# Performance work log

Hardware: AMD Instinct MI355X
Metric: run time of the kernel (lower is better)

The kernel has to match this reference:

```python
import jax, jax.numpy as jnp
import numpy as np

V = 32000   # vocab_size
D = 1024    # dim
NH = 16     # n_heads
HD = 64     # head_dim
L = 2       # n_layers
E = 8       # n_experts
K = 2       # n_active_experts
H = 2048    # expert_dim
B = 2
T = 1024
EPS = 1e-6
THETA = 10000.0
STD = 0.02


def rmsnorm(x, w):
    rms = jax.lax.rsqrt(jnp.mean(x * x, axis=-1, keepdims=True) + EPS)
    return x * rms * w


def rope_cos_sin(t_len):
    inv = 1.0 / (THETA ** (jnp.arange(0, HD, 2, dtype=jnp.float32) / HD))
    t = jnp.arange(t_len, dtype=jnp.float32)
    f = jnp.outer(t, inv)  # [T, HD//2]
    return jnp.cos(f), jnp.sin(f)


def apply_rope(x, cos, sin):
    # x: [B, T, NH, HD]; complex rotation on interleaved (even, odd) pairs
    xr = x[..., 0::2]
    xi = x[..., 1::2]
    c = cos[None, :, None, :]
    s = sin[None, :, None, :]
    out_r = xr * c - xi * s
    out_i = xr * s + xi * c
    return jnp.stack([out_r, out_i], axis=-1).reshape(x.shape)


def setup_inputs() -> dict:
    key = jax.random.key(0)
    ks = jax.random.split(key, 13)
    n = lambda k, shp: (jax.random.normal(k, shp, dtype=jnp.float32) * STD)
    return {
        "tokens": jax.random.randint(ks[0], (B, T), 0, V, dtype=jnp.int64)
                   if jax.config.jax_enable_x64 else
                   jax.random.randint(ks[0], (B, T), 0, V, dtype=jnp.int32),
        "emb": n(ks[1], (V, D)),            # tied embedding / output projection
        "attn_norm_w": jnp.ones((L, D), jnp.float32),
        "wq": n(ks[2], (L, D, D)),
        "wk": n(ks[3], (L, D, D)),
        "wv": n(ks[4], (L, D, D)),
        "wo": n(ks[5], (L, D, D)),
        "ffn_norm_w": jnp.ones((L, D), jnp.float32),
        "gate_w": n(ks[6], (L, D, E)),
        "w1": n(ks[7], (L, E, D, H)),
        "w2": n(ks[8], (L, E, H, D)),
        "w3": n(ks[9], (L, E, D, H)),
        "final_norm_w": jnp.ones((D,), jnp.float32),
    }


def reference(tokens, emb, attn_norm_w, wq, wk, wv, wo, ffn_norm_w,
              gate_w, w1, w2, w3, final_norm_w):
    b, t = tokens.shape
    h = emb[tokens]                                     # [B,T,D]
    cos, sin = rope_cos_sin(t)
    mask = jnp.where(jnp.tril(jnp.ones((t, t), bool)), 0.0, -jnp.inf)
    scale = 1.0 / np.sqrt(HD).astype(np.float32)
    aux_total = jnp.float32(0.0)

    for l in range(L):
        x = h
        # --- attention ---
        hn = rmsnorm(x, attn_norm_w[l])
        q = (hn @ wq[l]).reshape(b, t, NH, HD)
        k = (hn @ wk[l]).reshape(b, t, NH, HD)
        v = (hn @ wv[l]).reshape(b, t, NH, HD)
        q = apply_rope(q, cos, sin)
        k = apply_rope(k, cos, sin)
        scores = jnp.einsum('bqhd,bkhd->bhqk', q, k) * scale + mask
        attn = jax.nn.softmax(scores, axis=-1)
        o = jnp.einsum('bhqk,bkhd->bqhd', attn, v).reshape(b, t, D) @ wo[l]
        x = x + o
        # --- MoE ---
        xf = rmsnorm(x, ffn_norm_w[l]).reshape(-1, D)   # [N,D]
        gate_logits = xf @ gate_w[l]                    # [N,E]
        probs = jax.nn.softmax(gate_logits, axis=-1)
        vals, idx = jax.lax.top_k(probs, K)             # [N,K]
        w = vals / (jnp.sum(vals, axis=-1, keepdims=True) + 1e-8)
        oh = jax.nn.one_hot(idx, E, dtype=jnp.float32)  # [N,K,E]
        combine = jnp.sum(oh * w[..., None], axis=1)    # [N,E]
        tokens_per_expert = oh.sum(axis=1).mean(axis=0)
        aux_total = aux_total + E * jnp.sum(tokens_per_expert * probs.mean(axis=0))
        h1 = jnp.einsum('nd,edh->neh', xf, w1[l])
        h3 = jnp.einsum('nd,edh->neh', xf, w3[l])
        eo = jnp.einsum('neh,ehd->ned', jax.nn.silu(h1) * h3, w2[l])
        moe_out = jnp.einsum('ned,ne->nd', eo, combine).reshape(b, t, D)
        h = x + moe_out

    logits = rmsnorm(h, final_norm_w) @ emb.T           # [B,T,V]
    return logits, aux_total
```

## Files before the change

kernel.cpp:

```cpp
#include <hip/hip_runtime.h>
#include <hip/hip_bf16.h>
#include <math.h>

#define D_MODEL 1024
#define NHEADS  16
#define HDIM    64
#define NEXP    8
#define FFH     2048
#define BATCH   2
#define SEQ     1024
#define NTOK    2048
#define VOCAB   32000
#define LDSS    40

typedef __attribute__((ext_vector_type(4))) float f32x4;
typedef __attribute__((ext_vector_type(2))) float f32x2;
typedef __attribute__((ext_vector_type(8))) _Float16 f16x8;
typedef __attribute__((ext_vector_type(4))) unsigned short u16x4;

#define TIER    4.8828125e-4f
#define DESCALE 2.44140625e-4f
#define INV_S   0.015625f
#define INV_M   7.62939453125e-6f

__device__ __forceinline__ unsigned short f2h(float x) {
    _Float16 h = (_Float16)x;
    union { _Float16 h; unsigned short u; } v; v.h = h; return v.u;
}
__device__ __forceinline__ float h2f(unsigned short u) {
    union { unsigned short u; _Float16 h; } v; v.u = u; return (float)v.h;
}
__device__ __forceinline__ void split2h(float x, unsigned short& h, unsigned short& m) {
    _Float16 hf = (_Float16)(x * 64.f);
    union { _Float16 h; unsigned short u; } a; a.h = hf;
    h = a.u;
    float r = x - (float)hf * INV_S;
    _Float16 mf = (_Float16)(r * 131072.f);
    union { _Float16 h; unsigned short u; } b; b.h = mf;
    m = b.u;
}

#define MFMAH(a, b, c) __builtin_amdgcn_mfma_f32_16x16x32_f16((a), (b), (c), 0, 0, 0)

#define PSA ((long)NTOK * D_MODEL)
#define PSW ((long)D_MODEL * D_MODEL)

__global__ __launch_bounds__(256) void rmsnorm_kernel(const float* __restrict__ x,
    const float* __restrict__ wt, unsigned short* __restrict__ out2)
{
    __shared__ float red[4];
    int n = blockIdx.x;
    int c = threadIdx.x << 2;
    f32x4 v = *(const f32x4*)(x + (long)n*D_MODEL + c);
    float ss = v.x*v.x + v.y*v.y + v.z*v.z + v.w*v.w;
    #pragma unroll
    for (int dd = 32; dd; dd >>= 1) ss += __shfl_xor(ss, dd);
    if ((threadIdx.x & 63) == 0) red[threadIdx.x >> 6] = ss;
    __syncthreads();
    float tot = red[0] + red[1] + red[2] + red[3];
    float rms = rsqrtf(tot * (1.f / D_MODEL) + 1e-6f);
    f32x4 wv = *(const f32x4*)(wt + c);
    f32x4 o = v * rms;
    o = o * wv;
    u16x4 hv, mv;
    #pragma unroll
    for (int j = 0; j < 4; j++) { unsigned short h,m; split2h(o[j],h,m); hv[j]=h; mv[j]=m; }
    long idx = (long)n*D_MODEL + c;
    *(u16x4*)(out2 + 0*PSA + idx) = hv;
    *(u16x4*)(out2 + 1*PSA + idx) = mv;
}

__global__ __launch_bounds__(256) void wsplitT_kernel(
    const float* __restrict__ wqs, const float* __restrict__ wks, const float* __restrict__ wvs,
    unsigned short* __restrict__ oq, unsigned short* __restrict__ ok, unsigned short* __restrict__ ov)
{
    __shared__ float t[64][65];
    int k0 = blockIdx.x*64, n0 = blockIdx.y*64, z = blockIdx.z;
    const float* src = (z==0) ? wqs : (z==1) ? wks : wvs;
    unsigned short* dst = (z==0) ? oq : (z==1) ? ok : ov;
    int tid = threadIdx.x;
    int a = tid & 63, g = tid >> 6;
    #pragma unroll 4
    for (int i = 0; i < 16; i++) {
        int k = g*16 + i;
        t[k][a] = src[(long)(k0+k)*D_MODEL + n0 + a];
    }
    __syncthreads();
    #pragma unroll 4
    for (int i = 0; i < 16; i++) {
        int n = g*16 + i;
        float v = t[a][n];
        unsigned short h,m; split2h(v,h,m);
        long idx = (long)(n0+n)*D_MODEL + k0 + a;
        dst[0*PSW + idx] = h;
        dst[1*PSW + idx] = m;
    }
}

__global__ __launch_bounds__(256, 4) void qkv_kernel(
    const unsigned short* __restrict__ A2,
    const unsigned short* __restrict__ Wq2, const unsigned short* __restrict__ Wk2,
    const unsigned short* __restrict__ Wv2,
    float* __restrict__ qf, float* __restrict__ kf, float* __restrict__ vf)
{
    __shared__ __align__(16) unsigned short As[2][64*LDSS];
    __shared__ __align__(16) unsigned short Bs[2][64*LDSS];
    int z = blockIdx.z;
    const unsigned short* B2 = (z==0) ? Wq2 : (z==1) ? Wk2 : Wv2;
    float* out = (z==0) ? qf : (z==1) ? kf : vf;
    int n0 = blockIdx.x*64, m0 = blockIdx.y*64;
    int tid = threadIdx.x, w = tid >> 6, lane = tid & 63;
    int wm = (w >> 1)*32, wn = (w & 1)*32;
    int lr = lane & 15, lg = lane >> 4;
    f32x4 zero = {0.f,0.f,0.f,0.f};
    f32x4 a0[2][2], a1[2][2];
    #pragma unroll
    for (int mi = 0; mi < 2; mi++)
        #pragma unroll
        for (int ni = 0; ni < 2; ni++) { a0[mi][ni] = zero; a1[mi][ni] = zero; }
    int rb = tid >> 3, kc = (tid & 7) << 2;

    for (int k0 = 0; k0 < D_MODEL; k0 += 32) {
        #pragma unroll
        for (int p = 0; p < 2; p++) {
            int r = p*32 + rb;
            #pragma unroll
            for (int s = 0; s < 2; s++) {
                *(u16x4*)&As[s][r*LDSS + kc] = *(const u16x4*)(A2 + s*PSA + (long)(m0+r)*D_MODEL + k0 + kc);
                *(u16x4*)&Bs[s][r*LDSS + kc] = *(const u16x4*)(B2 + s*PSW + (long)(n0+r)*D_MODEL + k0 + kc);
            }
        }
        __syncthreads();
        f16x8 bh[2], bm[2];
        #pragma unroll
        for (int ni = 0; ni < 2; ni++) {
            bh[ni] = *(const f16x8*)&Bs[0][(wn + ni*16 + lr)*LDSS + lg*8];
            bm[ni] = *(const f16x8*)&Bs[1][(wn + ni*16 + lr)*LDSS + lg*8];
        }
        #pragma unroll
        for (int mi = 0; mi < 2; mi++) {
            f16x8 ah = *(const f16x8*)&As[0][(wm + mi*16 + lr)*LDSS + lg*8];
            f16x8 am = *(const f16x8*)&As[1][(wm + mi*16 + lr)*LDSS + lg*8];
            #pragma unroll
            for (int ni = 0; ni < 2; ni++) {
                a0[mi][ni] = MFMAH(ah, bh[ni], a0[mi][ni]);
                a1[mi][ni] = MFMAH(ah, bm[ni], a1[mi][ni]);
                a1[mi][ni] = MFMAH(am, bh[ni], a1[mi][ni]);
            }
        }
        __syncthreads();
    }
    #pragma unroll
    for (int mi = 0; mi < 2; mi++)
        #pragma unroll
        for (int r = 0; r < 4; r++) {
            long row = m0 + wm + mi*16 + lg*4 + r;
            #pragma unroll
            for (int ni = 0; ni < 2; ni++) {
                int col = n0 + wn + ni*16 + lr;
                out[row*D_MODEL + col] = (a0[mi][ni][r] + a1[mi][ni][r]*TIER) * DESCALE;
            }
        }
}

__global__ __launch_bounds__(256, 3) void wo_kernel(
    const float* __restrict__ A, const float* __restrict__ B, float* h)
{
    __shared__ __align__(16) unsigned short As[2][64*LDSS];
    __shared__ __align__(16) unsigned short Bs[2][64*LDSS];
    int n0 = blockIdx.x*64, m0 = blockIdx.y*64;
    int tid = threadIdx.x, w = tid >> 6, lane = tid & 63;
    int wm = (w >> 1)*32, wn = (w & 1)*32;
    int lr = lane & 15, lg = lane >> 4;
    f32x4 zero = {0.f,0.f,0.f,0.f};
    f32x4 a0[2][2], a1[2][2];
    #pragma unroll
    for (int mi = 0; mi < 2; mi++)
        #pragma unroll
        for (int ni = 0; ni < 2; ni++) { a0[mi][ni] = zero; a1[mi][ni] = zero; }
    int rb = tid >> 3, kc = (tid & 7) << 2;
    int nb = (tid & 31) << 1, kb = (tid >> 5) << 2;

    f32x4 pAv[2];
    f32x2 pBv[4];
    #pragma unroll
    for (int p = 0; p < 2; p++)
        pAv[p] = *(const f32x4*)(A + (long)(m0 + p*32 + rb)*D_MODEL + kc);
    #pragma unroll
    for (int i = 0; i < 4; i++)
        pBv[i] = *(const f32x2*)(B + (long)(kb + i)*D_MODEL + n0 + nb);

    for (int k0 = 0; k0 < D_MODEL; k0 += 32) {
        int kn = k0 + 32;
        #pragma unroll
        for (int p = 0; p < 2; p++) {
            int r = p*32 + rb;
            u16x4 hv, mv;
            #pragma unroll
            for (int j = 0; j < 4; j++) { unsigned short hh,mm; split2h(pAv[p][j],hh,mm); hv[j]=hh; mv[j]=mm; }
            *(u16x4*)&As[0][r*LDSS + kc] = hv;
            *(u16x4*)&As[1][r*LDSS + kc] = mv;
        }
        #pragma unroll
        for (int i = 0; i < 2; i++) {
            int r = nb + i;
            u16x4 hv, mv;
            unsigned short hh,mm;
            split2h(pBv[0][i],hh,mm); hv[0]=hh; mv[0]=mm;
            split2h(pBv[1][i],hh,mm); hv[1]=hh; mv[1]=mm;
            split2h(pBv[2][i],hh,mm); hv[2]=hh; mv[2]=mm;
            split2h(pBv[3][i],hh,mm); hv[3]=hh; mv[3]=mm;
            *(u16x4*)&Bs[0][r*LDSS + kb] = hv;
            *(u16x4*)&Bs[1][r*LDSS + kb] = mv;
        }
        if (kn < D_MODEL) {
            #pragma unroll
            for (int p = 0; p < 2; p++)
                pAv[p] = *(const f32x4*)(A + (long)(m0 + p*32 + rb)*D_MODEL + kn + kc);
            #pragma unroll
            for (int i = 0; i < 4; i++)
                pBv[i] = *(const f32x2*)(B + (long)(kn + kb + i)*D_MODEL + n0 + nb);
        }
        __syncthreads();
        f16x8 bh[2], bm[2];
        #pragma unroll
        for (int ni = 0; ni < 2; ni++) {
            bh[ni] = *(const f16x8*)&Bs[0][(wn + ni*16 + lr)*LDSS + lg*8];
            bm[ni] = *(const f16x8*)&Bs[1][(wn + ni*16 + lr)*LDSS + lg*8];
        }
        #pragma unroll
        for (int mi = 0; mi < 2; mi++) {
            f16x8 ah = *(const f16x8*)&As[0][(wm + mi*16 + lr)*LDSS + lg*8];
            f16x8 am = *(const f16x8*)&As[1][(wm + mi*16 + lr)*LDSS + lg*8];
            #pragma unroll
            for (int ni = 0; ni < 2; ni++) {
                a0[mi][ni] = MFMAH(ah, bh[ni], a0[mi][ni]);
                a1[mi][ni] = MFMAH(ah, bm[ni], a1[mi][ni]);
                a1[mi][ni] = MFMAH(am, bh[ni], a1[mi][ni]);
            }
        }
        __syncthreads();
    }
    #pragma unroll
    for (int mi = 0; mi < 2; mi++)
        #pragma unroll
        for (int r = 0; r < 4; r++) {
            long row = m0 + wm + mi*16 + lg*4 + r;
            #pragma unroll
            for (int ni = 0; ni < 2; ni++) {
                int col = n0 + wn + ni*16 + lr;
                h[row*D_MODEL + col] += (a0[mi][ni][r] + a1[mi][ni][r]*TIER) * DESCALE;
            }
        }
}

template<int SPL>
__global__ __launch_bounds__(256, 3) void moe13_kernel(
    const unsigned short* __restrict__ A2, const float* __restrict__ W1,
    const float* __restrict__ W3, float* __restrict__ G,
    const int* __restrict__ rowidx, const int* __restrict__ counts,
    const int* __restrict__ offsets)
{
    __shared__ __align__(16) unsigned short As[SPL][64*LDSS];
    __shared__ __align__(16) unsigned short Bs[SPL][128*LDSS];
    const int P1 = (SPL == 2) ? 1 : 0;
    int e = blockIdx.z;
    int cnt = counts[e], off = offsets[e];
    int n0 = blockIdx.x*128, m0 = blockIdx.y*64;
    if (m0 >= cnt) return;
    int tid = threadIdx.x, w = tid >> 6, lane = tid & 63;
    int wm = (w >> 1)*32, wn = (w & 1)*64;
    int lr = lane & 15, lg = lane >> 4;
    int rb = tid >> 3, kc = (tid & 7) << 2;
    f32x4 zero = {0.f,0.f,0.f,0.f};

    long arow[2]; int av[2];
    #pragma unroll
    for (int p = 0; p < 2; p++) {
        int r = p*32 + rb;
        av[p] = (m0 + r < cnt) ? 1 : 0;
        arow[p] = av[p] ? (long)rowidx[off + m0 + r] : 0;
    }
    u16x4 z4 = {0,0,0,0};
    f32x4 sl[2][4];

    #pragma unroll
    for (int mat = 0; mat < 2; mat++) {
        const float* bp = (mat ? W3 : W1) + (long)e * (D_MODEL*FFH);
        f32x4 a0[2][4], a1t[2][4];
        #pragma unroll
        for (int mi = 0; mi < 2; mi++)
            #pragma unroll
            for (int ni = 0; ni < 4; ni++) { a0[mi][ni] = zero; a1t[mi][ni] = zero; }

        for (int k0 = 0; k0 < D_MODEL; k0 += 32) {
            #pragma unroll
            for (int p = 0; p < 2; p++) {
                int r = p*32 + rb;
                #pragma unroll
                for (int s = 0; s < SPL; s++)
                    *(u16x4*)&As[s][r*LDSS + kc] = av[p] ?
                        *(const u16x4*)(A2 + s*PSA + arow[p]*D_MODEL + k0 + kc) : z4;
            }
            f32x4 c0 = *(const f32x4*)(bp + (long)(k0+kc+0)*FFH + n0 + rb*4);
            f32x4 c1 = *(const f32x4*)(bp + (long)(k0+kc+1)*FFH + n0 + rb*4);
            f32x4 c2 = *(const f32x4*)(bp + (long)(k0+kc+2)*FFH + n0 + rb*4);
            f32x4 c3 = *(const f32x4*)(bp + (long)(k0+kc+3)*FFH + n0 + rb*4);
            #pragma unroll
            for (int i = 0; i < 4; i++) {
                int r = rb*4 + i;
                if (SPL == 2) {
                    u16x4 hv, mv;
                    unsigned short hh,mm;
                    split2h(c0[i],hh,mm); hv[0]=hh; mv[0]=mm;
                    split2h(c1[i],hh,mm); hv[1]=hh; mv[1]=mm;
                    split2h(c2[i],hh,mm); hv[2]=hh; mv[2]=mm;
                    split2h(c3[i],hh,mm); hv[3]=hh; mv[3]=mm;
                    *(u16x4*)&Bs[0][r*LDSS + kc] = hv;
                    *(u16x4*)&Bs[P1][r*LDSS + kc] = mv;
                } else {
                    u16x4 hv = {f2h(c0[i]), f2h(c1[i]), f2h(c2[i]), f2h(c3[i])};
                    *(u16x4*)&Bs[0][r*LDSS + kc] = hv;
                }
            }
            __syncthreads();
            f16x8 bh[4], bm[4];
            #pragma unroll
            for (int ni = 0; ni < 4; ni++) {
                bh[ni] = *(const f16x8*)&Bs[0][(wn + ni*16 + lr)*LDSS + lg*8];
                if (SPL == 2) bm[ni] = *(const f16x8*)&Bs[P1][(wn + ni*16 + lr)*LDSS + lg*8];
            }
            #pragma unroll
            for (int mi = 0; mi < 2; mi++) {
                f16x8 ah = *(const f16x8*)&As[0][(wm + mi*16 + lr)*LDSS + lg*8];
                #pragma unroll
                for (int ni = 0; ni < 4; ni++) {
                    a0[mi][ni] = MFMAH(ah, bh[ni], a0[mi][ni]);
                    if (SPL == 2) {
                        f16x8 am = *(const f16x8*)&As[P1][(wm + mi*16 + lr)*LDSS + lg*8];
                        a1t[mi][ni] = MFMAH(ah, bm[ni], a1t[mi][ni]);
                        a1t[mi][ni] = MFMAH(am, bh[ni], a1t[mi][ni]);
                    }
                }
            }
            __syncthreads();
        }
        if (mat == 0) {
            #pragma unroll
            for (int mi = 0; mi < 2; mi++)
                #pragma unroll
                for (int ni = 0; ni < 4; ni++) {
                    f32x4 v = (SPL == 2) ? (a0[mi][ni] + a1t[mi][ni]*TIER)*DESCALE
                                         : a0[mi][ni]*INV_S;
                    #pragma unroll
                    for (int r = 0; r < 4; r++) {
                        float s = v[r];
                        v[r] = s / (1.f + expf(-s));
                    }
                    sl[mi][ni] = v;
                }
        } else {
            #pragma unroll
            for (int mi = 0; mi < 2; mi++)
                #pragma unroll
                for (int r = 0; r < 4; r++) {
                    int rowl = wm + mi*16 + lg*4 + r;
                    if (m0 + rowl < cnt) {
                        long crow = off + m0 + rowl;
                        #pragma unroll
                        for (int ni = 0; ni < 4; ni++) {
                            int col = n0 + wn + ni*16 + lr;
                            float v3 = (SPL == 2) ? (a0[mi][ni][r] + a1t[mi][ni][r]*TIER)*DESCALE
                                                  : a0[mi][ni][r]*INV_S;
                            G[crow*FFH + col] = sl[mi][ni][r] * v3;
                        }
                    }
                }
        }
    }
}

template<int SPL>
__global__ __launch_bounds__(256, 4) void w2_kernel(
    const float* __restrict__ G, const float* __restrict__ W2, float* h,
    const int* __restrict__ rowidx, const float* __restrict__ wrow,
    const int* __restrict__ counts, const int* __restrict__ offsets)
{
    __shared__ __align__(16) unsigned short As[SPL][64*LDSS];
    __shared__ __align__(16) unsigned short Bs[SPL][64*LDSS];
    const int P1 = (SPL == 2) ? 1 : 0;
    int e = blockIdx.z;
    int cnt = counts[e], off = offsets[e];
    int n0 = blockIdx.x*64, m0 = blockIdx.y*64;
    if (m0 >= cnt) return;
    const float* bp = W2 + (long)e * (FFH*D_MODEL);
    int tid = threadIdx.x, w = tid >> 6, lane = tid & 63;
    int wm = (w >> 1)*32, wn = (w & 1)*32;
    int lr = lane & 15, lg = lane >> 4;
    f32x4 zero = {0.f,0.f,0.f,0.f};
    f32x4 a0[2][2], a1[2][2];
    #pragma unroll
    for (int mi = 0; mi < 2; mi++)
        #pragma unroll
        for (int ni = 0; ni < 2; ni++) { a0[mi][ni] = zero; a1[mi][ni] = zero; }
    int rb = tid >> 3, kc = (tid & 7) << 2;
    int nb = (tid & 31) << 1, kb = (tid >> 5) << 2;

    int av[2];
    #pragma unroll
    for (int p = 0; p < 2; p++) av[p] = (m0 + p*32 + rb < cnt) ? 1 : 0;
    f32x4 pG[2];
    f32x2 pW[4];
    #pragma unroll
    for (int p = 0; p < 2; p++)
        pG[p] = av[p] ? *(const f32x4*)(G + (long)(off + m0 + p*32 + rb)*FFH + kc) : zero;
    #pragma unroll
    for (int i = 0; i < 4; i++)
        pW[i] = *(const f32x2*)(bp + (long)(kb + i)*D_MODEL + n0 + nb);

    for (int k0 = 0; k0 < FFH; k0 += 32) {
        int kn = k0 + 32;
        #pragma unroll
        for (int p = 0; p < 2; p++) {
            int r = p*32 + rb;
            if (SPL == 2) {
                u16x4 hv, mv;
                #pragma unroll
                for (int j = 0; j < 4; j++) { unsigned short hh,mm; split2h(pG[p][j],hh,mm); hv[j]=hh; mv[j]=mm; }
                *(u16x4*)&As[0][r*LDSS + kc] = hv;
                *(u16x4*)&As[P1][r*LDSS + kc] = mv;
            } else {
                u16x4 hv;
                #pragma unroll
                for (int j = 0; j < 4; j++) hv[j] = f2h(pG[p][j]);
                *(u16x4*)&As[0][r*LDSS + kc] = hv;
            }
        }
        #pragma unroll
        for (int i = 0; i < 2; i++) {
            int r = nb + i;
            if (SPL == 2) {
                u16x4 hv, mv;
                unsigned short hh,mm;
                split2h(pW[0][i],hh,mm); hv[0]=hh; mv[0]=mm;
                split2h(pW[1][i],hh,mm); hv[1]=hh; mv[1]=mm;
                split2h(pW[2][i],hh,mm); hv[2]=hh; mv[2]=mm;
                split2h(pW[3][i],hh,mm); hv[3]=hh; mv[3]=mm;
                *(u16x4*)&Bs[0][r*LDSS + kb] = hv;
                *(u16x4*)&Bs[P1][r*LDSS + kb] = mv;
            } else {
                u16x4 hv = {f2h(pW[0][i]), f2h(pW[1][i]), f2h(pW[2][i]), f2h(pW[3][i])};
                *(u16x4*)&Bs[0][r*LDSS + kb] = hv;
            }
        }
        if (kn < FFH) {
            #pragma unroll
            for (int p = 0; p < 2; p++)
                pG[p] = av[p] ? *(const f32x4*)(G + (long)(off + m0 + p*32 + rb)*FFH + kn + kc) : zero;
            #pragma unroll
            for (int i = 0; i < 4; i++)
                pW[i] = *(const f32x2*)(bp + (long)(kn + kb + i)*D_MODEL + n0 + nb);
        }
        __syncthreads();
        f16x8 bh[2], bm[2];
        #pragma unroll
        for (int ni = 0; ni < 2; ni++) {
            bh[ni] = *(const f16x8*)&Bs[0][(wn + ni*16 + lr)*LDSS + lg*8];
            if (SPL == 2) bm[ni] = *(const f16x8*)&Bs[P1][(wn + ni*16 + lr)*LDSS + lg*8];
        }
        #pragma unroll
        for (int mi = 0; mi < 2; mi++) {
            f16x8 ah = *(const f16x8*)&As[0][(wm + mi*16 + lr)*LDSS + lg*8];
            #pragma unroll
            for (int ni = 0; ni < 2; ni++) {
                a0[mi][ni] = MFMAH(ah, bh[ni], a0[mi][ni]);
                if (SPL == 2) {
                    f16x8 am = *(const f16x8*)&As[P1][(wm + mi*16 + lr)*LDSS + lg*8];
                    a1[mi][ni] = MFMAH(ah, bm[ni], a1[mi][ni]);
                    a1[mi][ni] = MFMAH(am, bh[ni], a1[mi][ni]);
                }
            }
        }
        __syncthreads();
    }
    #pragma unroll
    for (int mi = 0; mi < 2; mi++)
        #pragma unroll
        for (int r = 0; r < 4; r++) {
            int rowl = wm + mi*16 + lg*4 + r;
            if (m0 + rowl < cnt) {
                long crow = off + m0 + rowl;
                long n = rowidx[crow];
                float wgt = wrow[crow];
                #pragma unroll
                for (int ni = 0; ni < 2; ni++) {
                    int col = n0 + wn + ni*16 + lr;
                    float val = (SPL == 2) ? (a0[mi][ni][r] + a1[mi][ni][r]*TIER)*DESCALE
                                           : a0[mi][ni][r];
                    atomicAdd(&h[n*D_MODEL + col], wgt * val);
                }
            }
        }
}

__global__ __launch_bounds__(256, 3) void attn_kernel(
    const float* __restrict__ q, const float* __restrict__ k,
    const float* __restrict__ v, float* __restrict__ att)
{
    __shared__ __align__(16) unsigned short Qs[2][64*72];
    __shared__ __align__(16) unsigned short KP[2][2560];
    __shared__ __align__(16) unsigned short Vt[2][2560];

    int qt = blockIdx.x, bh = blockIdx.y;
    int b = bh >> 4, hh = bh & 15;
    int tid = threadIdx.x, w = tid >> 6, lane = tid & 63;
    int lr = lane & 15, lg = lane >> 4;
    int lrow = tid >> 4;
    int lcol = (tid & 15) << 2;

    const float* qbase = q + ((long)(b*SEQ + qt*64) * D_MODEL + hh*64);
    #pragma unroll
    for (int p = 0; p < 4; p++) {
        int r = p*16 + lrow;
        f32x4 vv = *(const f32x4*)(qbase + (long)r * D_MODEL + lcol);
        #pragma unroll
        for (int jj = 0; jj < 4; jj++) {
            unsigned short hh2,mm2; split2h(vv[jj],hh2,mm2);
            Qs[0][r*72 + lcol + jj] = hh2;
            Qs[1][r*72 + lcol + jj] = mm2;
        }
    }

    f32x4 zero = {0.f,0.f,0.f,0.f};
    f32x4 o0[4] = {zero, zero, zero, zero};
    f32x4 o1[4] = {zero, zero, zero, zero};
    float mrun[4] = {-INFINITY,-INFINITY,-INFINITY,-INFINITY};
    float lrun[4] = {0.f,0.f,0.f,0.f};

    int ntile = 2*qt + 2;
    for (int jt = 0; jt < ntile; jt++) {
        const float* kbase = k + ((long)(b*SEQ + jt*32) * D_MODEL + hh*64);
        const float* vbase = v + ((long)(b*SEQ + jt*32) * D_MODEL + hh*64);
        #pragma unroll
        for (int p = 0; p < 2; p++) {
            int r = p*16 + lrow;
            f32x4 kv4 = *(const f32x4*)(kbase + (long)r * D_MODEL + lcol);
            f32x4 vv4 = *(const f32x4*)(vbase + (long)r * D_MODEL + lcol);
            #pragma unroll
            for (int jj = 0; jj < 4; jj++) {
                unsigned short hh2,mm2;
                split2h(kv4[jj],hh2,mm2);
                KP[0][r*72 + lcol + jj] = hh2;
                KP[1][r*72 + lcol + jj] = mm2;
                split2h(vv4[jj],hh2,mm2);
                Vt[0][(lcol+jj)*40 + r] = hh2;
                Vt[1][(lcol+jj)*40 + r] = mm2;
            }
        }
        __syncthreads();

        f32x4 s0[2] = {zero, zero};
        f32x4 s1[2] = {zero, zero};
        #pragma unroll
        for (int ks = 0; ks < 2; ks++) {
            f16x8 qh = *(const f16x8*)&Qs[0][(w*16 + lr)*72 + ks*32 + lg*8];
            f16x8 qm = *(const f16x8*)&Qs[1][(w*16 + lr)*72 + ks*32 + lg*8];
            #pragma unroll
            for (int ni = 0; ni < 2; ni++) {
                f16x8 kh = *(const f16x8*)&KP[0][(ni*16 + lr)*72 + ks*32 + lg*8];
                f16x8 km = *(const f16x8*)&KP[1][(ni*16 + lr)*72 + ks*32 + lg*8];
                s0[ni] = MFMAH(qh, kh, s0[ni]);
                s1[ni] = MFMAH(qh, km, s1[ni]);
                s1[ni] = MFMAH(qm, kh, s1[ni]);
            }
        }
        __syncthreads();

        #pragma unroll
        for (int r = 0; r < 4; r++) {
            int qg = qt*64 + w*16 + lg*4 + r;
            float sv[2];
            float mx = -INFINITY;
            #pragma unroll
            for (int ni = 0; ni < 2; ni++) {
                int kg = jt*32 + ni*16 + lr;
                float val = (s0[ni][r] + s1[ni][r]*TIER) * (0.125f * DESCALE);
                if (kg > qg) val = -INFINITY;
                sv[ni] = val;
                mx = fmaxf(mx, val);
            }
            #pragma unroll
            for (int dd = 1; dd < 16; dd <<= 1)
                mx = fmaxf(mx, __shfl_xor(mx, dd));
            float mnew  = fmaxf(mrun[r], mx);
            float alpha = expf(mrun[r] - mnew);
            float ps = 0.f;
            #pragma unroll
            for (int ni = 0; ni < 2; ni++) {
                float pv = expf(sv[ni] - mnew);
                sv[ni] = pv;
                ps += pv;
            }
            #pragma unroll
            for (int dd = 1; dd < 16; dd <<= 1)
                ps += __shfl_xor(ps, dd);
            lrun[r] = lrun[r] * alpha + ps;
            mrun[r] = mnew;
            #pragma unroll
            for (int d = 0; d < 4; d++) { o0[d][r] *= alpha; o1[d][r] *= alpha; }
            int prow = w*16 + lg*4 + r;
            #pragma unroll
            for (int ni = 0; ni < 2; ni++) {
                unsigned short hh2,mm2; split2h(sv[ni],hh2,mm2);
                KP[0][prow*40 + ni*16 + lr] = hh2;
                KP[1][prow*40 + ni*16 + lr] = mm2;
            }
        }
        {
            f16x8 ph = *(const f16x8*)&KP[0][(w*16 + lr)*40 + lg*8];
            f16x8 pm = *(const f16x8*)&KP[1][(w*16 + lr)*40 + lg*8];
            #pragma unroll
            for (int ni = 0; ni < 4; ni++) {
                f16x8 vh = *(const f16x8*)&Vt[0][(ni*16 + lr)*40 + lg*8];
                f16x8 vm = *(const f16x8*)&Vt[1][(ni*16 + lr)*40 + lg*8];
                o0[ni] = MFMAH(ph, vh, o0[ni]);
                o1[ni] = MFMAH(ph, vm, o1[ni]);
                o1[ni] = MFMAH(pm, vh, o1[ni]);
            }
        }
        __syncthreads();
    }
    float* obase = att + ((long)(b*SEQ + qt*64) * D_MODEL + hh*64);
    #pragma unroll
    for (int r = 0; r < 4; r++) {
        float inv = DESCALE / lrun[r];
        #pragma unroll
        for (int ni = 0; ni < 4; ni++)
            obase[(long)(w*16 + lg*4 + r) * D_MODEL + ni*16 + lr] =
                (o0[ni][r] + o1[ni][r]*TIER) * inv;
    }
}

__global__ __launch_bounds__(256) void logits_kernel(
    const unsigned short* __restrict__ A0, const float* __restrict__ Bmat, float* __restrict__ C)
{
    __shared__ __align__(16) unsigned short As[128*LDSS];
    __shared__ __align__(16) unsigned short Bs[128*LDSS];
    int n0 = blockIdx.y * 128;
    int m0 = blockIdx.x * 128;
    int tid = threadIdx.x, w = tid >> 6, lane = tid & 63;
    int wm = (w >> 1)*64, wn = (w & 1)*64;
    int lr = lane & 15, lg = lane >> 4;
    f32x4 zero = {0.f,0.f,0.f,0.f};
    f32x4 acc[4][4];
    #pragma unroll
    for (int mi = 0; mi < 4; mi++)
        #pragma unroll
        for (int ni = 0; ni < 4; ni++) acc[mi][ni] = zero;
    int rb = tid >> 3, kc = (tid & 7) << 2;
    for (int k0 = 0; k0 < D_MODEL; k0 += 32) {
        #pragma unroll
        for (int p = 0; p < 4; p++) {
            int r = p*32 + rb;
            *(u16x4*)&As[r*LDSS + kc] = *(const u16x4*)(A0 + (long)(m0+r)*D_MODEL + k0 + kc);
            f32x4 vv = *(const f32x4*)(Bmat + (long)(n0+r)*D_MODEL + k0 + kc);
            u16x4 hv;
            #pragma unroll
            for (int j = 0; j < 4; j++) hv[j] = f2h(vv[j]);
            *(u16x4*)&Bs[r*LDSS + kc] = hv;
        }
        __syncthreads();
        f16x8 bfv[4], af[4];
        #pragma unroll
        for (int ni = 0; ni < 4; ni++)
            bfv[ni] = *(const f16x8*)&Bs[(wn + ni*16 + lr)*LDSS + lg*8];
        #pragma unroll
        for (int mi = 0; mi < 4; mi++)
            af[mi] = *(const f16x8*)&As[(wm + mi*16 + lr)*LDSS + lg*8];
        #pragma unroll
        for (int mi = 0; mi < 4; mi++)
            #pragma unroll
            for (int ni = 0; ni < 4; ni++)
                acc[mi][ni] = MFMAH(af[mi], bfv[ni], acc[mi][ni]);
        __syncthreads();
    }
    #pragma unroll
    for (int mi = 0; mi < 4; mi++)
        #pragma unroll
        for (int r = 0; r < 4; r++) {
            long row = m0 + wm + mi*16 + lg*4 + r;
            #pragma unroll
            for (int ni = 0; ni < 4; ni++) {
                int col = n0 + wn + ni*16 + lr;
                C[row*VOCAB + col] = acc[mi][ni][r] * INV_S;
            }
        }
}

__global__ __launch_bounds__(256) void embed_kernel(const int* __restrict__ tok,
    const float* __restrict__ emb, float* __restrict__ h)
{
    int n = blockIdx.x;
    int c = threadIdx.x << 2;
    long t = tok[n];
    *(f32x4*)(h + (long)n*D_MODEL + c) = *(const f32x4*)(emb + t*D_MODEL + c);
}

__global__ __launch_bounds__(256) void ropetab_kernel(float* __restrict__ tab)
{
    int idx = blockIdx.x * 256 + threadIdx.x;
    if (idx >= SEQ * 32) return;
    int t = idx >> 5, i = idx & 31;
    double inv = pow(10000.0, -(double)(2*i) / 64.0);
    double ang = (double)t * inv;
    tab[idx*2]   = (float)cos(ang);
    tab[idx*2+1] = (float)sin(ang);
}

__global__ __launch_bounds__(256) void rope_kernel(float* __restrict__ q, float* __restrict__ kk,
    const float* __restrict__ tab)
{
    int gid = blockIdx.x * 256 + threadIdx.x;
    if (gid >= NTOK * 512) return;
    int n   = gid >> 9;
    int rem = gid & 511;
    int hh  = rem >> 5;
    int i   = rem & 31;
    int t   = n & (SEQ - 1);
    float cs = tab[(t*32 + i)*2];
    float sn = tab[(t*32 + i)*2 + 1];
    long base = (long)n * D_MODEL + hh*64 + 2*i;
    float qr = q[base], qi = q[base+1];
    q[base]   = qr*cs - qi*sn;
    q[base+1] = qr*sn + qi*cs;
    float kr = kk[base], ki = kk[base+1];
    kk[base]   = kr*cs - ki*sn;
    kk[base+1] = kr*sn + ki*cs;
}

__global__ __launch_bounds__(64) void gate_kernel(const unsigned short* __restrict__ xf2,
    const float* __restrict__ gw, int* __restrict__ counts,
    int* __restrict__ eid, float* __restrict__ wts, float* __restrict__ pbuf)
{
    int n = blockIdx.x;
    int lane = threadIdx.x;
    float acc[8] = {0,0,0,0,0,0,0,0};
    for (int d0 = lane*4; d0 < D_MODEL; d0 += 256) {
        long idx = (long)n*D_MODEL + d0;
        u16x4 xh = *(const u16x4*)(xf2 + 0*PSA + idx);
        u16x4 xm = *(const u16x4*)(xf2 + 1*PSA + idx);
        #pragma unroll
        for (int j = 0; j < 4; j++) {
            float xv = h2f(xh[j])*INV_S + h2f(xm[j])*INV_M;
            const float* g = gw + (d0+j) * 8;
            #pragma unroll
            for (int e = 0; e < 8; e++) acc[e] += xv * g[e];
        }
    }
    #pragma unroll
    for (int e = 0; e < 8; e++) {
        #pragma unroll
        for (int dd = 32; dd; dd >>= 1) acc[e] += __shfl_xor(acc[e], dd);
    }
    if (lane == 0) {
        float mx = acc[0];
        #pragma unroll
        for (int e = 1; e < 8; e++) mx = fmaxf(mx, acc[e]);
        float pe[8], ssum = 0.f;
        #pragma unroll
        for (int e = 0; e < 8; e++) { pe[e] = expf(acc[e] - mx); ssum += pe[e]; }
        float sinv = 1.f / ssum;
        #pragma unroll
        for (int e = 0; e < 8; e++) { pe[e] *= sinv; pbuf[n*8 + e] = pe[e]; }
        int e1 = 0;
        #pragma unroll
        for (int e = 1; e < 8; e++) if (pe[e] > pe[e1]) e1 = e;
        int e2 = -1;
        #pragma unroll
        for (int e = 0; e < 8; e++) if (e != e1 && (e2 < 0 || pe[e] > pe[e2])) e2 = e;
        float v1 = pe[e1], v2 = pe[e2];
        float wsum = v1 + v2 + 1e-8f;
        eid[n*2] = e1; eid[n*2+1] = e2;
        wts[n*2] = v1 / wsum; wts[n*2+1] = v2 / wsum;
        atomicAdd(counts + e1, 1);
        atomicAdd(counts + e2, 1);
    }
}

__global__ __launch_bounds__(64) void scan_kernel(const int* __restrict__ counts,
    int* __restrict__ offs, int* __restrict__ cursor,
    const float* __restrict__ pbuf, float* __restrict__ aux)
{
    int t = threadIdx.x;
    int e = t & 7, c = t >> 3;
    float s = 0.f;
    for (int n = 0; n < NTOK/8; n++)
        s += pbuf[(c*(NTOK/8) + n)*8 + e];
    #pragma unroll
    for (int dd = 8; dd < 64; dd <<= 1) s += __shfl_xor(s, dd);
    __shared__ float red[8];
    if (t < 8) red[t] = s;
    __syncthreads();
    if (t == 0) {
        int o = 0; float a = 0.f;
        for (int kk = 0; kk < 8; kk++) {
            offs[kk] = o; cursor[kk] = o; o += counts[kk];
            a += (float)counts[kk] * red[kk];
        }
        aux[0] += 8.f * a / ((float)NTOK * (float)NTOK);
    }
}

__global__ __launch_bounds__(256) void assign_kernel(const int* __restrict__ eid,
    const float* __restrict__ wts, int* __restrict__ cursor,
    int* __restrict__ rowidx, float* __restrict__ wrow)
{
    int n = blockIdx.x * 256 + threadIdx.x;
    if (n >= NTOK) return;
    #pragma unroll
    for (int s = 0; s < 2; s++) {
        int e = eid[n*2 + s];
        int p = atomicAdd(cursor + e, 1);
        rowidx[p] = n;
        wrow[p] = wts[n*2 + s];
    }
}

__global__ void write_aux_kernel(float* __restrict__ out, const float* __restrict__ aux)
{
    if (threadIdx.x == 0 && blockIdx.x == 0)
        out[(long)NTOK * VOCAB] = aux[0];
}

extern "C" void kernel_launch(void* const* d_in, const int* in_sizes, int n_in,
                              void* d_out, int out_size, void* d_ws, size_t ws_size,
                              hipStream_t stream)
{
    const int*   tokens = (const int*)d_in[0];
    const float* emb    = (const float*)d_in[1];
    const float* anw    = (const float*)d_in[2];
    const float* wq     = (const float*)d_in[3];
    const float* wk     = (const float*)d_in[4];
    const float* wv     = (const float*)d_in[5];
    const float* wo     = (const float*)d_in[6];
    const float* fnw    = (const float*)d_in[7];
    const float* gw     = (const float*)d_in[8];
    const float* w1     = (const float*)d_in[9];
    const float* w2     = (const float*)d_in[10];
    const float* w3     = (const float*)d_in[11];
    const float* finw   = (const float*)d_in[12];
    float* out = (float*)d_out;

    char* W = (char*)d_ws;
    const size_t MB = 1024u * 1024u;
    int*   counts = (int*)(W + 0);
    int*   offs   = (int*)(W + 64);
    int*   cursor = (int*)(W + 128);
    float* aux    = (float*)(W + 192);
    int*   eid    = (int*)(W + 4096);
    float* wts    = (float*)(W + 4096 + 16384);
    int*   rowix  = (int*)(W + 4096 + 32768);
    float* wrow   = (float*)(W + 4096 + 49152);
    float* pbuf   = (float*)(W + 4096 + 65536);
    float* rtab   = (float*)(W + 4096 + 131072 + 65536);
    float*          h    = (float*)(W + 1*MB);
    unsigned short* hn2  = (unsigned short*)(W + 9*MB);
    float*          qf   = (float*)(W + 17*MB);
    float*          kf   = (float*)(W + 25*MB);
    float*          vf   = (float*)(W + 33*MB);
    unsigned short* wq2  = (unsigned short*)(W + 41*MB);
    unsigned short* wk2  = (unsigned short*)(W + 45*MB);
    unsigned short* wv2  = (unsigned short*)(W + 49*MB);
    float*          att  = (float*)(W + 41*MB);
    float*          g    = (float*)(W + 17*MB);

    hipMemsetAsync(W, 0, 256, stream);
    ropetab_kernel<<<(SEQ*32 + 255)/256, 256, 0, stream>>>(rtab);
    embed_kernel<<<NTOK, 256, 0, stream>>>(tokens, emb, h);

    for (int l = 0; l < 2; l++) {
        const float* wql = wq + (size_t)l*D_MODEL*D_MODEL;
        const float* wkl = wk + (size_t)l*D_MODEL*D_MODEL;
        const float* wvl = wv + (size_t)l*D_MODEL*D_MODEL;
        const float* wol = wo + (size_t)l*D_MODEL*D_MODEL;

        rmsnorm_kernel<<<NTOK, 256, 0, stream>>>(h, anw + (size_t)l*D_MODEL, hn2);
        wsplitT_kernel<<<dim3(16, 16, 3), 256, 0, stream>>>(wql, wkl, wvl, wq2, wk2, wv2);
        qkv_kernel<<<dim3(D_MODEL/64, NTOK/64, 3), 256, 0, stream>>>(hn2, wq2, wk2, wv2, qf, kf, vf);
        rope_kernel<<<(NTOK*512 + 255)/256, 256, 0, stream>>>(qf, kf, rtab);
        attn_kernel<<<dim3(SEQ/64, BATCH*NHEADS), 256, 0, stream>>>(qf, kf, vf, att);
        wo_kernel<<<dim3(D_MODEL/64, NTOK/64), 256, 0, stream>>>(att, wol, h);

        rmsnorm_kernel<<<NTOK, 256, 0, stream>>>(h, fnw + (size_t)l*D_MODEL, hn2);
        hipMemsetAsync(W, 0, 160, stream);
        gate_kernel<<<NTOK, 64, 0, stream>>>(hn2, gw + (size_t)l*D_MODEL*NEXP, counts, eid, wts, pbuf);
        scan_kernel<<<1, 64, 0, stream>>>(counts, offs, cursor, pbuf, aux);
        assign_kernel<<<(NTOK + 255)/256, 256, 0, stream>>>(eid, wts, cursor, rowix, wrow);

        const float* w1l = w1 + (size_t)l*NEXP*D_MODEL*FFH;
        const float* w3l = w3 + (size_t)l*NEXP*D_MODEL*FFH;
        const float* w2l = w2 + (size_t)l*NEXP*FFH*D_MODEL;
        dim3 g13(FFH/128, 2*NTOK/64, NEXP);
        dim3 g2d(D_MODEL/64, 2*NTOK/64, NEXP);
        if (l == 0) {
            moe13_kernel<2><<<g13, 256, 0, stream>>>(hn2, w1l, w3l, g, rowix, counts, offs);
            w2_kernel<2><<<g2d, 256, 0, stream>>>(g, w2l, h, rowix, wrow, counts, offs);
        } else {
            moe13_kernel<1><<<g13, 256, 0, stream>>>(hn2, w1l, w3l, g, rowix, counts, offs);
            w2_kernel<1><<<g2d, 256, 0, stream>>>(g, w2l, h, rowix, wrow, counts, offs);
        }
    }

    rmsnorm_kernel<<<NTOK, 256, 0, stream>>>(h, finw, hn2);
    logits_kernel<<<dim3(NTOK/128, VOCAB/128), 256, 0, stream>>>(hn2, emb, out);
    write_aux_kernel<<<1, 1, 0, stream>>>(out, aux);
}
```

Baseline: 1.740 ms.

## Prefetch next K-tile into registers in MoE W1/W3 GEMM and raise occupancy bounds

The MoE up-projection kernel now issues global loads for the next K-slice of activations and expert weights into registers before the current slice's MFMA work. This lets memory latency overlap with compute. Launch-bounds minimum blocks are also raised for the qkv and moe13 kernels to push the compiler toward more resident waves. The register prefetch buffers raise register pressure, and the higher occupancy target may force spills.

```diff
diff --git a/kernel.cpp b/kernel.cpp
--- a/kernel.cpp
+++ b/kernel.cpp
@@ -97,7 +97,7 @@
     }
 }
 
-__global__ __launch_bounds__(256, 4) void qkv_kernel(
+__global__ __launch_bounds__(256, 6) void qkv_kernel(
     const unsigned short* __restrict__ A2,
     const unsigned short* __restrict__ Wq2, const unsigned short* __restrict__ Wk2,
     const unsigned short* __restrict__ Wv2,
@@ -255,7 +255,7 @@
 }
 
 template<int SPL>
-__global__ __launch_bounds__(256, 3) void moe13_kernel(
+__global__ __launch_bounds__(256, 4) void moe13_kernel(
     const unsigned short* __restrict__ A2, const float* __restrict__ W1,
     const float* __restrict__ W3, float* __restrict__ G,
     const int* __restrict__ rowidx, const int* __restrict__ counts,
@@ -293,35 +293,50 @@
             #pragma unroll
             for (int ni = 0; ni < 4; ni++) { a0[mi][ni] = zero; a1t[mi][ni] = zero; }
 
+        u16x4 pA[2][SPL];
+        f32x4 pB[4];
+        #pragma unroll
+        for (int p = 0; p < 2; p++)
+            #pragma unroll
+            for (int s = 0; s < SPL; s++)
+                pA[p][s] = av[p] ? *(const u16x4*)(A2 + s*PSA + arow[p]*D_MODEL + kc) : z4;
+        #pragma unroll
+        for (int i = 0; i < 4; i++)
+            pB[i] = *(const f32x4*)(bp + (long)(kc + i)*FFH + n0 + rb*4);
+
         for (int k0 = 0; k0 < D_MODEL; k0 += 32) {
-            #pragma unroll
-            for (int p = 0; p < 2; p++) {
-                int r = p*32 + rb;
+            int kn = k0 + 32;
+            #pragma unroll
+            for (int p = 0; p < 2; p++)
                 #pragma unroll
                 for (int s = 0; s < SPL; s++)
-                    *(u16x4*)&As[s][r*LDSS + kc] = av[p] ?
-                        *(const u16x4*)(A2 + s*PSA + arow[p]*D_MODEL + k0 + kc) : z4;
-            }
-            f32x4 c0 = *(const f32x4*)(bp + (long)(k0+kc+0)*FFH + n0 + rb*4);
-            f32x4 c1 = *(const f32x4*)(bp + (long)(k0+kc+1)*FFH + n0 + rb*4);
-            f32x4 c2 = *(const f32x4*)(bp + (long)(k0+kc+2)*FFH + n0 + rb*4);
-            f32x4 c3 = *(const f32x4*)(bp + (long)(k0+kc+3)*FFH + n0 + rb*4);
+                    *(u16x4*)&As[s][(p*32 + rb)*LDSS + kc] = pA[p][s];
             #pragma unroll
             for (int i = 0; i < 4; i++) {
                 int r = rb*4 + i;
                 if (SPL == 2) {
                     u16x4 hv, mv;
                     unsigned short hh,mm;
-                    split2h(c0[i],hh,mm); hv[0]=hh; mv[0]=mm;
-                    split2h(c1[i],hh,mm); hv[1]=hh; mv[1]=mm;
-                    split2h(c2[i],hh,mm); hv[2]=hh; mv[2]=mm;
-                    split2h(c3[i],hh,mm); hv[3]=hh; mv[3]=mm;
+                    split2h(pB[0][i],hh,mm); hv[0]=hh; mv[0]=mm;
+                    split2h(pB[1][i],hh,mm); hv[1]=hh; mv[1]=mm;
+                    split2h(pB[2][i],hh,mm); hv[2]=hh; mv[2]=mm;
+                    split2h(pB[3][i],hh,mm); hv[3]=hh; mv[3]=mm;
                     *(u16x4*)&Bs[0][r*LDSS + kc] = hv;
                     *(u16x4*)&Bs[P1][r*LDSS + kc] = mv;
                 } else {
-                    u16x4 hv = {f2h(c0[i]), f2h(c1[i]), f2h(c2[i]), f2h(c3[i])};
+                    u16x4 hv = {f2h(pB[0][i]), f2h(pB[1][i]), f2h(pB[2][i]), f2h(pB[3][i])};
                     *(u16x4*)&Bs[0][r*LDSS + kc] = hv;
                 }
+            }
+            if (kn < D_MODEL) {
+                #pragma unroll
+                for (int p = 0; p < 2; p++)
+                    #pragma unroll
+                    for (int s = 0; s < SPL; s++)
+                        pA[p][s] = av[p] ? *(const u16x4*)(A2 + s*PSA + arow[p]*D_MODEL + kn + kc) : z4;
+                #pragma unroll
+                for (int i = 0; i < 4; i++)
+                    pB[i] = *(const f32x4*)(bp + (long)(kn + kc + i)*FFH + n0 + rb*4);
             }
             __syncthreads();
             f16x8 bh[4], bm[4];
```

Result: slower. 2.827 ms (+62.5%).

## Load A operand fragments directly from global into registers, bypassing LDS

Applied to the files above, without the earlier changes.

In the qkv, MoE up-projection and logits GEMMs, the A-operand tile is no longer staged through shared memory. Each wave loads its MFMA fragments straight from global memory into registers, which removes the LDS writes and reads for A and shrinks shared memory use. The MoE kernel's launch bound is also raised to 4 blocks per SM. The cost is that A rows are now fetched redundantly by the waves sharing them, with less coalesced 16-byte-per-lane loads that lean on the L2 cache.

```diff
diff --git a/kernel.cpp b/kernel.cpp
--- a/kernel.cpp
+++ b/kernel.cpp
@@ -103,7 +103,6 @@
     const unsigned short* __restrict__ Wv2,
     float* __restrict__ qf, float* __restrict__ kf, float* __restrict__ vf)
 {
-    __shared__ __align__(16) unsigned short As[2][64*LDSS];
     __shared__ __align__(16) unsigned short Bs[2][64*LDSS];
     int z = blockIdx.z;
     const unsigned short* B2 = (z==0) ? Wq2 : (z==1) ? Wk2 : Wv2;
@@ -119,17 +118,22 @@
         #pragma unroll
         for (int ni = 0; ni < 2; ni++) { a0[mi][ni] = zero; a1[mi][ni] = zero; }
     int rb = tid >> 3, kc = (tid & 7) << 2;
+    long arow0 = (long)(m0 + wm + lr) * D_MODEL;
+    long arow1 = (long)(m0 + wm + 16 + lr) * D_MODEL;
 
     for (int k0 = 0; k0 < D_MODEL; k0 += 32) {
         #pragma unroll
         for (int p = 0; p < 2; p++) {
             int r = p*32 + rb;
             #pragma unroll
-            for (int s = 0; s < 2; s++) {
-                *(u16x4*)&As[s][r*LDSS + kc] = *(const u16x4*)(A2 + s*PSA + (long)(m0+r)*D_MODEL + k0 + kc);
+            for (int s = 0; s < 2; s++)
                 *(u16x4*)&Bs[s][r*LDSS + kc] = *(const u16x4*)(B2 + s*PSW + (long)(n0+r)*D_MODEL + k0 + kc);
-            }
-        }
+        }
+        f16x8 ah[2], am[2];
+        ah[0] = *(const f16x8*)(A2 + 0*PSA + arow0 + k0 + lg*8);
+        ah[1] = *(const f16x8*)(A2 + 0*PSA + arow1 + k0 + lg*8);
+        am[0] = *(const f16x8*)(A2 + 1*PSA + arow0 + k0 + lg*8);
+        am[1] = *(const f16x8*)(A2 + 1*PSA + arow1 + k0 + lg*8);
         __syncthreads();
         f16x8 bh[2], bm[2];
         #pragma unroll
@@ -138,16 +142,13 @@
             bm[ni] = *(const f16x8*)&Bs[1][(wn + ni*16 + lr)*LDSS + lg*8];
         }
         #pragma unroll
-        for (int mi = 0; mi < 2; mi++) {
-            f16x8 ah = *(const f16x8*)&As[0][(wm + mi*16 + lr)*LDSS + lg*8];
-            f16x8 am = *(const f16x8*)&As[1][(wm + mi*16 + lr)*LDSS + lg*8];
+        for (int mi = 0; mi < 2; mi++)
             #pragma unroll
             for (int ni = 0; ni < 2; ni++) {
-                a0[mi][ni] = MFMAH(ah, bh[ni], a0[mi][ni]);
-                a1[mi][ni] = MFMAH(ah, bm[ni], a1[mi][ni]);
-                a1[mi][ni] = MFMAH(am, bh[ni], a1[mi][ni]);
-            }
-        }
+                a0[mi][ni] = MFMAH(ah[mi], bh[ni], a0[mi][ni]);
+                a1[mi][ni] = MFMAH(ah[mi], bm[ni], a1[mi][ni]);
+                a1[mi][ni] = MFMAH(am[mi], bh[ni], a1[mi][ni]);
+            }
         __syncthreads();
     }
     #pragma unroll
@@ -255,13 +256,12 @@
 }
 
 template<int SPL>
-__global__ __launch_bounds__(256, 3) void moe13_kernel(
+__global__ __launch_bounds__(256, 4) void moe13_kernel(
     const unsigned short* __restrict__ A2, const float* __restrict__ W1,
     const float* __restrict__ W3, float* __restrict__ G,
     const int* __restrict__ rowidx, const int* __restrict__ counts,
     const int* __restrict__ offsets)
 {
-    __shared__ __align__(16) unsigned short As[SPL][64*LDSS];
     __shared__ __align__(16) unsigned short Bs[SPL][128*LDSS];
     const int P1 = (SPL == 2) ? 1 : 0;
     int e = blockIdx.z;
@@ -273,15 +273,15 @@
     int lr = lane & 15, lg = lane >> 4;
     int rb = tid >> 3, kc = (tid & 7) << 2;
     f32x4 zero = {0.f,0.f,0.f,0.f};
-
-    long arow[2]; int av[2];
-    #pragma unroll
-    for (int p = 0; p < 2; p++) {
-        int r = p*32 + rb;
-        av[p] = (m0 + r < cnt) ? 1 : 0;
-        arow[p] = av[p] ? (long)rowidx[off + m0 + r] : 0;
-    }
-    u16x4 z4 = {0,0,0,0};
+    f16x8 zf = {(_Float16)0,(_Float16)0,(_Float16)0,(_Float16)0,(_Float16)0,(_Float16)0,(_Float16)0,(_Float16)0};
+
+    long arowf[2]; int avf[2];
+    #pragma unroll
+    for (int mi = 0; mi < 2; mi++) {
+        int rowl = m0 + wm + mi*16 + lr;
+        avf[mi] = (rowl < cnt) ? 1 : 0;
+        arowf[mi] = avf[mi] ? (long)rowidx[off + rowl] * D_MODEL : 0;
+    }
     f32x4 sl[2][4];
 
     #pragma unroll
@@ -294,14 +294,6 @@
             for (int ni = 0; ni < 4; ni++) { a0[mi][ni] = zero; a1t[mi][ni] = zero; }
 
         for (int k0 = 0; k0 < D_MODEL; k0 += 32) {
-            #pragma unroll
-            for (int p = 0; p < 2; p++) {
-                int r = p*32 + rb;
-                #pragma unroll
-                for (int s = 0; s < SPL; s++)
-                    *(u16x4*)&As[s][r*LDSS + kc] = av[p] ?
-                        *(const u16x4*)(A2 + s*PSA + arow[p]*D_MODEL + k0 + kc) : z4;
-            }
             f32x4 c0 = *(const f32x4*)(bp + (long)(k0+kc+0)*FFH + n0 + rb*4);
             f32x4 c1 = *(const f32x4*)(bp + (long)(k0+kc+1)*FFH + n0 + rb*4);
             f32x4 c2 = *(const f32x4*)(bp + (long)(k0+kc+2)*FFH + n0 + rb*4);
@@ -323,6 +315,13 @@
                     *(u16x4*)&Bs[0][r*LDSS + kc] = hv;
                 }
             }
+            f16x8 ah[2], am[2];
+            #pragma unroll
+            for (int mi = 0; mi < 2; mi++) {
+                ah[mi] = avf[mi] ? *(const f16x8*)(A2 + 0*PSA + arowf[mi] + k0 + lg*8) : zf;
+                if (SPL == 2)
+                    am[mi] = avf[mi] ? *(const f16x8*)(A2 + 1*PSA + arowf[mi] + k0 + lg*8) : zf;
+            }
             __syncthreads();
             f16x8 bh[4], bm[4];
             #pragma unroll
@@ -331,18 +330,15 @@
                 if (SPL == 2) bm[ni] = *(const f16x8*)&Bs[P1][(wn + ni*16 + lr)*LDSS + lg*8];
             }
             #pragma unroll
-            for (int mi = 0; mi < 2; mi++) {
-                f16x8 ah = *(const f16x8*)&As[0][(wm + mi*16 + lr)*LDSS + lg*8];
+            for (int mi = 0; mi < 2; mi++)
                 #pragma unroll
                 for (int ni = 0; ni < 4; ni++) {
-                    a0[mi][ni] = MFMAH(ah, bh[ni], a0[mi][ni]);
+                    a0[mi][ni] = MFMAH(ah[mi], bh[ni], a0[mi][ni]);
                     if (SPL == 2) {
-                        f16x8 am = *(const f16x8*)&As[P1][(wm + mi*16 + lr)*LDSS + lg*8];
-                        a1t[mi][ni] = MFMAH(ah, bm[ni], a1t[mi][ni]);
-                        a1t[mi][ni] = MFMAH(am, bh[ni], a1t[mi][ni]);
+                        a1t[mi][ni] = MFMAH(ah[mi], bm[ni], a1t[mi][ni]);
+                        a1t[mi][ni] = MFMAH(am[mi], bh[ni], a1t[mi][ni]);
                     }
                 }
-            }
             __syncthreads();
         }
         if (mat == 0) {
@@ -644,7 +640,6 @@
 __global__ __launch_bounds__(256) void logits_kernel(
     const unsigned short* __restrict__ A0, const float* __restrict__ Bmat, float* __restrict__ C)
 {
-    __shared__ __align__(16) unsigned short As[128*LDSS];
     __shared__ __align__(16) unsigned short Bs[128*LDSS];
     int n0 = blockIdx.y * 128;
     int m0 = blockIdx.x * 128;
@@ -658,25 +653,26 @@
         #pragma unroll
         for (int ni = 0; ni < 4; ni++) acc[mi][ni] = zero;
     int rb = tid >> 3, kc = (tid & 7) << 2;
+    long abase = (long)(m0 + wm + lr) * D_MODEL;
     for (int k0 = 0; k0 < D_MODEL; k0 += 32) {
         #pragma unroll
         for (int p = 0; p < 4; p++) {
             int r = p*32 + rb;
-            *(u16x4*)&As[r*LDSS + kc] = *(const u16x4*)(A0 + (long)(m0+r)*D_MODEL + k0 + kc);
             f32x4 vv = *(const f32x4*)(Bmat + (long)(n0+r)*D_MODEL + k0 + kc);
             u16x4 hv;
             #pragma unroll
             for (int j = 0; j < 4; j++) hv[j] = f2h(vv[j]);
             *(u16x4*)&Bs[r*LDSS + kc] = hv;
         }
-        __syncthreads();
-        f16x8 bfv[4], af[4];
+        f16x8 af[4];
+        #pragma unroll
+        for (int mi = 0; mi < 4; mi++)
+            af[mi] = *(const f16x8*)(A0 + abase + (long)mi*16*D_MODEL + k0 + lg*8);
+        __syncthreads();
+        f16x8 bfv[4];
         #pragma unroll
         for (int ni = 0; ni < 4; ni++)
             bfv[ni] = *(const f16x8*)&Bs[(wn + ni*16 + lr)*LDSS + lg*8];
-        #pragma unroll
-        for (int mi = 0; mi < 4; mi++)
-            af[mi] = *(const f16x8*)&As[(wm + mi*16 + lr)*LDSS + lg*8];
         #pragma unroll
         for (int mi = 0; mi < 4; mi++)
             #pragma unroll
```

Result: slower. 2.365 ms (+35.9%).
